# Kernel tuning notes

Hardware: AMD Instinct MI355X
Metric: run time of the kernel (lower is better)

## Reference

```python
import jax, jax.numpy as jnp
import numpy as np

N = 524288
NUM_LEVELS = 16
FEATS = 2
LOG2_T = 19
TABLE = 1 << LOG2_T
MIN_RES, MAX_RES = 16, 1024
PRIMES = np.array([1, 2654435761, 805459861], dtype=np.uint32)
_growth = np.exp((np.log(MAX_RES) - np.log(MIN_RES)) / (NUM_LEVELS - 1))
SCALINGS = np.floor(MIN_RES * _growth ** np.arange(NUM_LEVELS)).astype(np.float32)  # [L]


def hash_encode(positions, table):
    # positions [N,3] in [0,1]; table [L*T, F]
    scaled = positions[:, None, :] * jnp.asarray(SCALINGS)[None, :, None]  # [N,L,3]
    fl = jnp.floor(scaled)
    ce = jnp.ceil(scaled)
    offset = scaled - fl  # [N,L,3]
    primes = jnp.asarray(PRIMES)  # [3] uint32
    lvl_off = jnp.arange(NUM_LEVELS, dtype=jnp.uint32) * jnp.uint32(TABLE)  # [L]
    out = jnp.zeros(scaled.shape[:2] + (FEATS,), scaled.dtype)
    for corner in range(8):
        bits = np.array([(corner >> d) & 1 for d in range(3)], dtype=np.float32)
        coord = jnp.where(jnp.asarray(bits, dtype=bool), ce, fl)
        h = coord.astype(jnp.int32).astype(jnp.uint32) * primes  # [N,L,3]
        h = h[..., 0] ^ h[..., 1] ^ h[..., 2]
        idx = ((h & jnp.uint32(TABLE - 1)) + lvl_off).astype(jnp.int32)  # [N,L]
        b = jnp.asarray(bits)
        w = jnp.prod(b * offset + (1.0 - b) * (1.0 - offset), axis=-1, keepdims=True)  # [N,L,1]
        out = out + w * table[idx]
    return out.reshape(out.shape[0], NUM_LEVELS * FEATS)  # [N,32]


def nerf_encode(d):
    # NeRFEncoding: 4 freqs in 2**linspace(0,4,4), include_input=True -> 27 dims
    freqs = 2.0 ** jnp.linspace(0.0, 4.0, 4)
    scaled = (2.0 * jnp.pi * d)[..., None] * freqs  # [N,3,4]
    scaled = scaled.reshape(d.shape[0], -1)  # [N,12]
    enc = jnp.sin(jnp.concatenate([scaled, scaled + jnp.pi / 2.0], axis=-1))  # [N,24]
    return jnp.concatenate([enc, d], axis=-1)  # [N,27]


def setup_inputs() -> dict:
    key = jax.random.key(0)
    ks = jax.random.split(key, 16)
    w = lambda k, i, o: jax.random.normal(k, (i, o), jnp.float32) * (1.0 / np.sqrt(i))
    return {
        "positions": jax.random.uniform(ks[0], (N, 3), jnp.float32),
        "directions": jax.random.normal(ks[1], (N, 3), jnp.float32),
        "hash_table": (jax.random.uniform(ks[2], (NUM_LEVELS * TABLE, FEATS), jnp.float32) * 2.0 - 1.0) * 1e-3,
        "w0": w(ks[3], 32, 64), "b0": jnp.zeros((64,), jnp.float32),
        "w1": w(ks[4], 64, 64), "b1": jnp.zeros((64,), jnp.float32),
        "w2": w(ks[5], 64, 64), "b2": jnp.zeros((64,), jnp.float32),
        "wr": w(ks[6], 91, 32), "br": jnp.zeros((32,), jnp.float32),
        "wc": w(ks[7], 32, 3), "bc": jnp.zeros((3,), jnp.float32),
        "wd": w(ks[8], 64, 1), "bd": jnp.zeros((1,), jnp.float32),
    }


def reference(positions, directions, hash_table, w0, b0, w1, b1, w2, b2, wr, br, wc, bc, wd, bd):
    enc_xyz = hash_encode(positions, hash_table)  # [N,32]
    enc_dir = nerf_encode(directions)  # [N,27]
    h = jax.nn.relu(enc_xyz @ w0 + b0)
    h = jax.nn.relu(h @ w1 + b1)
    base = h @ w2 + b2  # [N,64], linear out (out_activation=None)
    rgb_h = jnp.concatenate([enc_dir, base], axis=-1) @ wr + br  # [N,32], single layer
    rgb = jax.nn.sigmoid(rgb_h @ wc + bc)  # [N,3]
    density = jax.nn.softplus(base @ wd + bd)  # [N,1]
    return jnp.concatenate([rgb, density], axis=-1)  # [N,4]
```

## Files before the change

kernel.cpp:

```cpp
#include <hip/hip_runtime.h>
#include <math.h>

#define NPTS 524288
#define LOG2T 19
#define TSIZE (1u << LOG2T)
#define TMASK (TSIZE - 1u)

typedef unsigned int uint32;
typedef unsigned short ushort16;

typedef __attribute__((ext_vector_type(8))) short short8;
typedef __attribute__((ext_vector_type(4))) float f32x4;

__device__ __forceinline__ float bf2f(ushort16 u) {
    union { uint32 i; float f; } v; v.i = ((uint32)u) << 16; return v.f;
}
__device__ __forceinline__ ushort16 f2bf(float f) {
    union { float f; uint32 i; } v; v.f = f;
    uint32 r = v.i + 0x7fffu + ((v.i >> 16) & 1u);
    return (ushort16)(r >> 16);
}
__device__ __forceinline__ uint32 pack2(float a, float b) {
    return (uint32)f2bf(a) | ((uint32)f2bf(b) << 16);
}
__device__ __forceinline__ float ldin(const void* p, int i, bool f32) {
    return f32 ? ((const float*)p)[i] : bf2f(((const ushort16*)p)[i]);
}

struct Scal16 { float s[16]; };
struct Freq4  { float f[4]; };
struct HashP  { float s[16]; int dD[8]; int doff[8]; };
struct DenseP { int dD[6]; int pfx[7]; };

__global__ __launch_bounds__(256) void k_cvt10(const void* __restrict__ pos,
                                               const float4* __restrict__ tbl,
                                               uint4* __restrict__ tbl2F) {
    __shared__ int sFlag;
    int tid = threadIdx.x;
    if (tid < 64) {
        const ushort16* ph = (const ushort16*)pos;
        float v0 = bf2f(ph[tid]), v1 = bf2f(ph[tid + 64]);
        bool odd = !(fabsf(v0) <= 4.f) || !(fabsf(v1) <= 4.f);
        unsigned long long m = __ballot(odd);
        if (tid == 0) sFlag = (m != 0ull) ? 1 : 0;
    }
    __syncthreads();
    if (sFlag == 0) return;
    size_t g = (size_t)blockIdx.x * 256 + tid;
    float4 v0 = tbl[(size_t)3 * TSIZE + 2 * g];
    float4 v1 = tbl[(size_t)3 * TSIZE + 2 * g + 1];
    uint4 o;
    o.x = pack2(v0.x, v0.y); o.y = pack2(v0.z, v0.w);
    o.z = pack2(v1.x, v1.y); o.w = pack2(v1.z, v1.w);
    tbl2F[g] = o;
}

__global__ __launch_bounds__(256) void k_dense(const void* __restrict__ pos,
                                               const void* __restrict__ tbl,
                                               uint4* __restrict__ dense4,
                                               DenseP dp) {
    __shared__ int sFlag;
    int tid = threadIdx.x;
    if (tid < 64) {
        const ushort16* ph = (const ushort16*)pos;
        float v0 = bf2f(ph[tid]), v1 = bf2f(ph[tid + 64]);
        bool odd = !(fabsf(v0) <= 4.f) || !(fabsf(v1) <= 4.f);
        unsigned long long m = __ballot(odd);
        if (tid == 0) sFlag = (m != 0ull) ? 1 : 0;
    }
    __syncthreads();
    const bool f32 = (sFlag != 0);

    int e = blockIdx.x * 256 + tid;
    if (e >= dp.pfx[6]) return;
    int l = 0;
#pragma unroll
    for (int k = 1; k < 6; ++k) l += (e >= dp.pfx[k]) ? 1 : 0;
    int c = e - dp.pfx[l];
    int D = dp.dD[l], D2 = D * D;
    int cz = c / D2; int rm = c - cz * D2;
    int cy = rm / D; int cx = rm - cy * D;

    uint32 base = (uint32)l << LOG2T;
    uint32 hz  = (uint32)cz * 805459861u;
    uint32 hy0 = (uint32)cy * 2654435761u;
    uint32 hy1 = (uint32)(cy + 1) * 2654435761u;
    uint32 h00 = ((((uint32)cx)       ^ hy0 ^ hz) & TMASK) + base;
    uint32 h10 = ((((uint32)(cx + 1)) ^ hy0 ^ hz) & TMASK) + base;
    uint32 h01 = ((((uint32)cx)       ^ hy1 ^ hz) & TMASK) + base;
    uint32 h11 = ((((uint32)(cx + 1)) ^ hy1 ^ hz) & TMASK) + base;

    uint4 o;
    if (f32) {
        const float2* t2 = (const float2*)tbl;
        float2 a = t2[h00], b = t2[h10], cc = t2[h01], d = t2[h11];
        o.x = pack2(a.x, a.y); o.y = pack2(b.x, b.y);
        o.z = pack2(cc.x, cc.y); o.w = pack2(d.x, d.y);
    } else {
        const uint32* t1 = (const uint32*)tbl;
        o.x = t1[h00]; o.y = t1[h10]; o.z = t1[h01]; o.w = t1[h11];
    }
    dense4[e] = o;
}

__global__ __launch_bounds__(256) void k_hashU(const void* __restrict__ pos,
                                               const void* __restrict__ tbl,
                                               const uint32* __restrict__ tbl2F,
                                               const uint4* __restrict__ dense4,
                                               uint32* __restrict__ enc,
                                               HashP hp, int lvl0) {
    __shared__ __align__(16) uint4 sPosQ[192];
    __shared__ int sFlag;
    int tid = threadIdx.x;
    if (tid < 64) {
        const ushort16* ph = (const ushort16*)pos;
        float v0 = bf2f(ph[tid]), v1 = bf2f(ph[tid + 64]);
        bool odd = !(fabsf(v0) <= 4.f) || !(fabsf(v1) <= 4.f);
        unsigned long long m = __ballot(odd);
        if (tid == 0) sFlag = (m != 0ull) ? 1 : 0;
    }
    __syncthreads();
    const bool f32 = (sFlag != 0);

    int lvl = lvl0 + (blockIdx.x & 7);
    int chunk = blockIdx.x >> 3;
    int p0 = chunk * 256;
    int pt = p0 + tid;

    {
        int n16 = f32 ? 192 : 96;
        const uint4* src = (const uint4*)((const char*)pos + (size_t)p0 * (f32 ? 12 : 6));
        for (int i = tid; i < n16; i += 256) sPosQ[i] = src[i];
    }
    __syncthreads();

    float x, y, z;
    if (f32) {
        const float* pf = (const float*)sPosQ;
        x = pf[3 * tid]; y = pf[3 * tid + 1]; z = pf[3 * tid + 2];
    } else {
        const ushort16* ph2 = (const ushort16*)sPosQ;
        x = bf2f(ph2[3 * tid]); y = bf2f(ph2[3 * tid + 1]); z = bf2f(ph2[3 * tid + 2]);
    }

    float s = hp.s[lvl];
    float sx = x * s, sy = y * s, sz = z * s;
    float fx = floorf(sx), fy = floorf(sy), fz = floorf(sz);
    float cx = ceilf(sx), cy = ceilf(sy), cz = ceilf(sz);
    float ox = sx - fx, oy = sy - fy, oz = sz - fz;
    float wx0 = 1.f - ox, wy0 = 1.f - oy, wz0 = 1.f - oz;

    float a0 = 0.f, a1 = 0.f;

    if (lvl < 6) {
        int D = hp.dD[lvl], D2 = D * D;
        int fxi = (int)fx, fyi = (int)fy, fzi = (int)fz;
        bool dxb = ((int)cx != fxi);
        bool dyb = ((int)cy != fyi);
        bool dzb = ((int)cz != fzi);
        const uint4* dp4 = dense4 + hp.doff[lvl];
        int i0 = fxi + fyi * D + fzi * D2;
        uint4 P0 = dp4[i0];
        uint4 P1 = dp4[i0 + (dzb ? D2 : 0)];
        {
            uint32 fv = P0.x, cv = dxb ? P0.y : P0.x;
            float w = wy0 * wz0;
            a0 += w * (wx0 * bf2f((ushort16)(fv & 0xffffu)) + ox * bf2f((ushort16)(cv & 0xffffu)));
            a1 += w * (wx0 * bf2f((ushort16)(fv >> 16))     + ox * bf2f((ushort16)(cv >> 16)));
        }
        {
            uint32 fv = dyb ? P0.z : P0.x;
            uint32 cv = dyb ? (dxb ? P0.w : P0.z) : (dxb ? P0.y : P0.x);
            float w = oy * wz0;
            a0 += w * (wx0 * bf2f((ushort16)(fv & 0xffffu)) + ox * bf2f((ushort16)(cv & 0xffffu)));
            a1 += w * (wx0 * bf2f((ushort16)(fv >> 16))     + ox * bf2f((ushort16)(cv >> 16)));
        }
        {
            uint32 fv = P1.x, cv = dxb ? P1.y : P1.x;
            float w = wy0 * oz;
            a0 += w * (wx0 * bf2f((ushort16)(fv & 0xffffu)) + ox * bf2f((ushort16)(cv & 0xffffu)));
            a1 += w * (wx0 * bf2f((ushort16)(fv >> 16))     + ox * bf2f((ushort16)(cv >> 16)));
        }
        {
            uint32 fv = dyb ? P1.z : P1.x;
            uint32 cv = dyb ? (dxb ? P1.w : P1.z) : (dxb ? P1.y : P1.x);
            float w = oy * oz;
            a0 += w * (wx0 * bf2f((ushort16)(fv & 0xffffu)) + ox * bf2f((ushort16)(cv & 0xffffu)));
            a1 += w * (wx0 * bf2f((ushort16)(fv >> 16))     + ox * bf2f((ushort16)(cv >> 16)));
        }
    } else {
        const uint32* tp; uint32 base;
        if (f32) { tp = tbl2F; base = (uint32)(lvl - 6) << LOG2T; }
        else     { tp = (const uint32*)tbl; base = (uint32)lvl << LOG2T; }
        uint32 hx0 = (uint32)(int)fx;
        uint32 hx1 = (uint32)(int)cx;
        uint32 hy0 = (uint32)(int)fy * 2654435761u;
        uint32 hy1 = (uint32)(int)cy * 2654435761u;
        uint32 hz0 = (uint32)(int)fz * 805459861u;
        uint32 hz1 = (uint32)(int)cz * 805459861u;
#pragma unroll
        for (int yz = 0; yz < 4; ++yz) {
            uint32 m = ((yz & 1) ? hy1 : hy0) ^ ((yz & 2) ? hz1 : hz0);
            float wyz = ((yz & 1) ? oy : wy0) * ((yz & 2) ? oz : wz0);
            uint32 i0 = ((hx0 ^ m) & TMASK) + base;
            uint32 i1 = ((hx1 ^ m) & TMASK) + base;
            uint32 d0, d1;
            if (i1 == (i0 ^ 1u)) {
                uint2 pv = *(const uint2*)(tp + (i0 & ~1u));
                d0 = (i0 & 1u) ? pv.y : pv.x;
                d1 = (i0 & 1u) ? pv.x : pv.y;
            } else {
                d0 = tp[i0]; d1 = tp[i1];
            }
            a0 += wyz * (wx0 * bf2f((ushort16)(d0 & 0xffffu)) + ox * bf2f((ushort16)(d1 & 0xffffu)));
            a1 += wyz * (wx0 * bf2f((ushort16)(d0 >> 16))     + ox * bf2f((ushort16)(d1 >> 16)));
        }
    }
    enc[(size_t)lvl * NPTS + pt] = pack2(a0, a1);
}

__global__ __launch_bounds__(256) void k_hash(const void* __restrict__ pos,
                                              const void* __restrict__ tbl,
                                              uint32* __restrict__ enc,
                                              Scal16 sc) {
    __shared__ int sFlag;
    int tid = threadIdx.x;
    if (tid < 64) {
        const ushort16* ph = (const ushort16*)pos;
        float v0 = bf2f(ph[tid]), v1 = bf2f(ph[tid + 64]);
        bool odd = !(fabsf(v0) <= 4.f) || !(fabsf(v1) <= 4.f);
        unsigned long long m = __ballot(odd);
        if (tid == 0) sFlag = (m != 0ull) ? 1 : 0;
    }
    __syncthreads();
    const bool f32 = (sFlag != 0);

    int lvl = ((blockIdx.x >> 14) << 3) + (blockIdx.x & 7);
    int pt = ((blockIdx.x >> 3) & 2047) * 256 + tid;

    float s = sc.s[lvl];
    float x = ldin(pos, 3 * pt, f32), y = ldin(pos, 3 * pt + 1, f32), z = ldin(pos, 3 * pt + 2, f32);
    float sx = x * s, sy = y * s, sz = z * s;
    float fx = floorf(sx), fy = floorf(sy), fz = floorf(sz);
    float cx = ceilf(sx), cy = ceilf(sy), cz = ceilf(sz);
    float ox = sx - fx, oy = sy - fy, oz = sz - fz;
    uint32 hx0 = (uint32)(int)fx;
    uint32 hx1 = (uint32)(int)cx;
    uint32 hy0 = (uint32)(int)fy * 2654435761u;
    uint32 hy1 = (uint32)(int)cy * 2654435761u;
    uint32 hz0 = (uint32)(int)fz * 805459861u;
    uint32 hz1 = (uint32)(int)cz * 805459861u;
    uint32 base = (uint32)lvl << LOG2T;
    float wx0 = 1.f - ox, wy0 = 1.f - oy, wz0 = 1.f - oz;

    float a0 = 0.f, a1 = 0.f;
    if (f32) {
        const float* tf = (const float*)tbl;
#pragma unroll
        for (int yz = 0; yz < 4; ++yz) {
            uint32 m = ((yz & 1) ? hy1 : hy0) ^ ((yz & 2) ? hz1 : hz0);
            float wyz = ((yz & 1) ? oy : wy0) * ((yz & 2) ? oz : wz0);
            uint32 i0 = ((hx0 ^ m) & TMASK) + base;
            uint32 i1 = ((hx1 ^ m) & TMASK) + base;
            float4 pv = *(const float4*)(tf + (size_t)(i0 & ~1u) * 2);
            bool lo = !(i0 & 1u);
            float f0 = lo ? pv.x : pv.z, f1 = lo ? pv.y : pv.w;
            float c0, c1;
            if (i1 == (i0 ^ 1u)) { c0 = lo ? pv.z : pv.x; c1 = lo ? pv.w : pv.y; }
            else { float2 tv = ((const float2*)tbl)[i1]; c0 = tv.x; c1 = tv.y; }
            a0 += wyz * (wx0 * f0 + ox * c0);
            a1 += wyz * (wx0 * f1 + ox * c1);
        }
    } else {
#pragma unroll
        for (int cr = 0; cr < 8; ++cr) {
            uint32 h = ((cr & 1) ? hx1 : hx0) ^ ((cr & 2) ? hy1 : hy0) ^ ((cr & 4) ? hz1 : hz0);
            uint32 idx = (h & TMASK) + base;
            uint32 dv = ((const uint32*)tbl)[idx];
            float w = ((cr & 1) ? ox : wx0) * ((cr & 2) ? oy : wy0) * ((cr & 4) ? oz : wz0);
            a0 += w * bf2f((ushort16)(dv & 0xffffu));
            a1 += w * bf2f((ushort16)(dv >> 16));
        }
    }
    enc[(size_t)lvl * NPTS + pt] = pack2(a0, a1);
}

#define STRY 72
#define STRW0 40
#define STRW12 72
#define STRWR 104
#define MSTRX 100
#define PPI 128
#define NIT (NPTS / PPI)

__global__ __launch_bounds__(512) void k_mlp(
    const void* __restrict__ pos,
    const uint32* __restrict__ enc, const void* __restrict__ dirs,
    const void* __restrict__ w0, const void* __restrict__ b0,
    const void* __restrict__ w1, const void* __restrict__ b1,
    const void* __restrict__ w2, const void* __restrict__ b2,
    const void* __restrict__ wr, const void* __restrict__ br,
    const void* __restrict__ wc, const void* __restrict__ bc,
    const void* __restrict__ wd, const void* __restrict__ bd,
    void* __restrict__ out, Freq4 fq)
{
    __shared__ __align__(16) ushort16 sX[PPI * MSTRX];
    __shared__ __align__(16) ushort16 sY[PPI * STRY];
    __shared__ __align__(16) ushort16 sW0[64 * STRW0];
    __shared__ __align__(16) ushort16 sW1[64 * STRW12];
    __shared__ __align__(16) ushort16 sW2[64 * STRW12];
    __shared__ __align__(16) ushort16 sWR[32 * STRWR];
    __shared__ __align__(16) ushort16 sW4[16 * STRWR];
    __shared__ __align__(16) float sB0[64], sB1[64], sB2[64], sBR[32], sFB[4];
    __shared__ int sFlag;

    int tid = threadIdx.x;

    if (tid < 64) {
        const ushort16* ph = (const ushort16*)pos;
        float v0 = bf2f(ph[tid]), v1 = bf2f(ph[tid + 64]);
        bool odd = !(fabsf(v0) <= 4.f) || !(fabsf(v1) <= 4.f);
        unsigned long long m = __ballot(odd);
        if (tid == 0) sFlag = (m != 0ull) ? 1 : 0;
    }
    __syncthreads();
    const bool f32 = (sFlag != 0);

    for (int i = tid; i < 2048; i += 512) { int k = i >> 6, n = i & 63; sW0[n * STRW0 + k] = f2bf(ldin(w0, i, f32)); }
    for (int i = tid; i < 4096; i += 512) { int k = i >> 6, n = i & 63; sW1[n * STRW12 + k] = f2bf(ldin(w1, i, f32)); }
    for (int i = tid; i < 4096; i += 512) { int k = i >> 6, n = i & 63; sW2[n * STRW12 + k] = f2bf(ldin(w2, i, f32)); }
    for (int i = tid; i < 2912; i += 512) {
        int r = i >> 5, n = i & 31; int k = (r < 27) ? r : r + 5;
        sWR[n * STRWR + k] = f2bf(ldin(wr, i, f32));
    }
    if (tid < 160) { int n = tid / 5, k = 27 + tid % 5; sWR[n * STRWR + k] = 0; }
    for (int i = tid; i < 1536; i += 512) {
        int n = i / 96, j = i % 96;
        float v = 0.f;
        if (n == 3 && j < 64) v = ldin(wd, j, f32);
        else if (n < 3 && j >= 64) v = ldin(wc, (j - 64) * 3 + n, f32);
        sW4[n * STRWR + j] = f2bf(v);
    }
    if (tid < 64) { sB0[tid] = ldin(b0, tid, f32); sB1[tid] = ldin(b1, tid, f32); sB2[tid] = ldin(b2, tid, f32); }
    if (tid < 32) sBR[tid] = ldin(br, tid, f32);
    if (tid < 3) sFB[tid] = ldin(bc, tid, f32);
    if (tid == 3) sFB[3] = ldin(bd, 0, f32);

    int lane = tid & 63, wv = tid >> 6;
    int colg = lane & 15, quad = lane >> 4;
    int myrow = wv * 16 + colg;

    for (int c = blockIdx.x; c < NIT; c += gridDim.x) {
        int p0 = c * PPI;
        __syncthreads();

        for (int i = tid; i < 1024; i += 512) {
            int l = i >> 6, p2 = (i & 63) * 2;
            uint2 e = *(const uint2*)&enc[(size_t)l * NPTS + p0 + p2];
            *(uint32*)&sX[p2 * MSTRX + 2 * l] = e.x;
            *(uint32*)&sX[(p2 + 1) * MSTRX + 2 * l] = e.y;
        }
        if (tid < 384) {
            int p = tid / 3, i2 = tid - 3 * (tid / 3);
            float dvv = ldin(dirs, 3 * (p0 + p) + i2, f32);
            ushort16* row = &sX[p * MSTRX + 64];
            float td = 6.28318530717958647692f * dvv;
            float a0 = td * fq.f[0], a1 = td * fq.f[1], a2 = td * fq.f[2], a3 = td * fq.f[3];
            uint2 sv, cv;
            sv.x = pack2(__sinf(a0), __sinf(a1));
// ... 211 lines not shown
                for (int r = 0; r < 4; ++r) {
                    float v = fmaxf(acc[r] + bias, 0.f);
                    sY[(wv * 16 + quad * 4 + r) * STRY + nt * 16 + colg] = f2bf(v);
                }
            }
        }
        __syncthreads();
        {
            short8 a0 = *(const short8*)&sY[(wv * 16 + colg) * STRY + quad * 8];
            short8 a1 = *(const short8*)&sY[(wv * 16 + colg) * STRY + 32 + quad * 8];
#pragma unroll
            for (int nt = 0; nt < 4; ++nt) {
                short8 bb0 = *(const short8*)&sW1[(nt * 16 + colg) * STRW12 + quad * 8];
                short8 bb1 = *(const short8*)&sW1[(nt * 16 + colg) * STRW12 + 32 + quad * 8];
                f32x4 acc = {0.f, 0.f, 0.f, 0.f};
                acc = __builtin_amdgcn_mfma_f32_16x16x32_bf16(a0, bb0, acc, 0, 0, 0);
                acc = __builtin_amdgcn_mfma_f32_16x16x32_bf16(a1, bb1, acc, 0, 0, 0);
                float bias = sB1[nt * 16 + colg];
#pragma unroll
                for (int r = 0; r < 4; ++r) {
                    float v = fmaxf(acc[r] + bias, 0.f);
                    sX[(wv * 16 + quad * 4 + r) * FSTRX + nt * 16 + colg] = f2bf(v);
                }
            }
        }
        __syncthreads();
        {
            short8 a0 = *(const short8*)&sX[(wv * 16 + colg) * FSTRX + quad * 8];
            short8 a1 = *(const short8*)&sX[(wv * 16 + colg) * FSTRX + 32 + quad * 8];
#pragma unroll
            for (int nt = 0; nt < 4; ++nt) {
                short8 bb0 = *(const short8*)&sW2[(nt * 16 + colg) * STRW12 + quad * 8];
                short8 bb1 = *(const short8*)&sW2[(nt * 16 + colg) * STRW12 + 32 + quad * 8];
                f32x4 acc = {0.f, 0.f, 0.f, 0.f};
                acc = __builtin_amdgcn_mfma_f32_16x16x32_bf16(a0, bb0, acc, 0, 0, 0);
                acc = __builtin_amdgcn_mfma_f32_16x16x32_bf16(a1, bb1, acc, 0, 0, 0);
                float bias = sB2[nt * 16 + colg];
#pragma unroll
                for (int r = 0; r < 4; ++r) {
                    sY[(wv * 16 + quad * 4 + r) * STRY + nt * 16 + colg] = f2bf(acc[r] + bias);
                }
            }
        }
        if (tid < 192) {
            int p = tid / 3, i2 = tid % 3;
            float dvv = ldin(dirs, 3 * (p0 + p) + i2, f32);
            ushort16* row = &sX[p * FSTRX + 64];
            float td = 6.28318530717958647692f * dvv;
#pragma unroll
            for (int j = 0; j < 4; ++j) {
                float arg = td * fq.f[j];
                float sv, cv;
                sincosf(arg, &sv, &cv);
                row[i2 * 4 + j] = f2bf(sv);
                row[12 + i2 * 4 + j] = f2bf(cv);
            }
            row[24 + i2] = f2bf(dvv);
        } else {
            int p = tid - 192;
            ushort16* row = &sX[p * FSTRX + 64];
#pragma unroll
            for (int j = 27; j < 32; ++j) row[j] = 0;
        }
        __syncthreads();
        {
            short8 a0 = *(const short8*)&sX[(wv * 16 + colg) * FSTRX + 64 + quad * 8];
            short8 a1 = *(const short8*)&sY[(wv * 16 + colg) * STRY + quad * 8];
            short8 a2 = *(const short8*)&sY[(wv * 16 + colg) * STRY + 32 + quad * 8];
#pragma unroll
            for (int nt = 0; nt < 2; ++nt) {
                short8 bb0 = *(const short8*)&sWR[(nt * 16 + colg) * STRWR + quad * 8];
                short8 bb1 = *(const short8*)&sWR[(nt * 16 + colg) * STRWR + 32 + quad * 8];
                short8 bb2 = *(const short8*)&sWR[(nt * 16 + colg) * STRWR + 64 + quad * 8];
                f32x4 acc = {0.f, 0.f, 0.f, 0.f};
                acc = __builtin_amdgcn_mfma_f32_16x16x32_bf16(a0, bb0, acc, 0, 0, 0);
                acc = __builtin_amdgcn_mfma_f32_16x16x32_bf16(a1, bb1, acc, 0, 0, 0);
                acc = __builtin_amdgcn_mfma_f32_16x16x32_bf16(a2, bb2, acc, 0, 0, 0);
                float bias = sBR[nt * 16 + colg];
#pragma unroll
                for (int r = 0; r < 4; ++r) {
                    sX[(wv * 16 + quad * 4 + r) * FSTRX + nt * 16 + colg] = f2bf(acc[r] + bias);
                }
            }
        }
        __syncthreads();
        if (tid < 64) {
            int pt = p0 + tid;
            float r0 = 0.f, r1 = 0.f, r2 = 0.f, dd = 0.f;
            const ushort16* hx = &sX[tid * FSTRX];
            const ushort16* hb = &sY[tid * STRY];
#pragma unroll
            for (int k = 0; k < 32; ++k) {
                float hv = bf2f(hx[k]);
                r0 += hv * sWCf[k * 3 + 0];
                r1 += hv * sWCf[k * 3 + 1];
                r2 += hv * sWCf[k * 3 + 2];
            }
#pragma unroll
            for (int k = 0; k < 64; ++k) dd += bf2f(hb[k]) * sWDf[k];
            r0 += sWCf[96]; r1 += sWCf[97]; r2 += sWCf[98]; dd += sWCf[99];
            r0 = 1.f / (1.f + expf(-r0));
            r1 = 1.f / (1.f + expf(-r1));
            r2 = 1.f / (1.f + expf(-r2));
            float sp = (dd > 0.f) ? (dd + log1pf(expf(-dd))) : log1pf(expf(dd));
            if (f32) {
                float4 o4; o4.x = r0; o4.y = r1; o4.z = r2; o4.w = sp;
                ((float4*)out)[pt] = o4;
            } else {
                uint2 o;
                o.x = pack2(r0, r1); o.y = pack2(r2, sp);
                ((uint2*)out)[pt] = o;
            }
        }
    }
}

extern "C" void kernel_launch(void* const* d_in, const int* in_sizes, int n_in,
                              void* d_out, int out_size, void* d_ws, size_t ws_size,
                              hipStream_t stream) {
    (void)in_sizes; (void)n_in; (void)out_size;

    Scal16 sc;
    double g = exp((log(1024.0) - log(16.0)) / 15.0);
    for (int l = 0; l < 16; ++l) sc.s[l] = (float)floor(16.0 * pow(g, (double)l));

    Freq4 fq;
    float lv[4] = {0.f, 4.f / 3.f, 8.f / 3.f, 4.f};
    for (int j = 0; j < 4; ++j) fq.f[j] = (float)pow(2.0, (double)lv[j]);

    DenseP dpp;
    HashP hp;
    dpp.pfx[0] = 0;
    for (int l = 0; l < 6; ++l) {
        int D = (int)sc.s[l] + 1;
        dpp.dD[l] = D;
        dpp.pfx[l + 1] = dpp.pfx[l] + D * D * D;
    }
    for (int l = 0; l < 16; ++l) hp.s[l] = sc.s[l];
    for (int l = 0; l < 8; ++l) {
        hp.dD[l]   = (l < 6) ? dpp.dD[l] : 1;
        hp.doff[l] = (l < 6) ? dpp.pfx[l] : 0;
    }
    int ndense = dpp.pfx[6];

    const size_t enc_bytes   = (size_t)16 * NPTS * 4;
    const size_t tbl2F_bytes = (size_t)10 * TSIZE * 4;
    const size_t dense_bytes = (size_t)ndense * 16 + 64;
    const size_t need_new = enc_bytes + tbl2F_bytes + dense_bytes;

    if (ws_size >= need_new) {
        uint32* enc   = (uint32*)d_ws;
        uint32* tbl2F = (uint32*)((char*)d_ws + enc_bytes);
        uint4*  dense4 = (uint4*)((char*)d_ws + enc_bytes + tbl2F_bytes);
        k_cvt10<<<dim3(5120), dim3(256), 0, stream>>>(d_in[0], (const float4*)d_in[2], (uint4*)tbl2F);
        k_dense<<<dim3((ndense + 255) / 256), dim3(256), 0, stream>>>(d_in[0], d_in[2], dense4, dpp);
        k_hashU<<<dim3(8 * NPTS / 256), dim3(256), 0, stream>>>(d_in[0], d_in[2], tbl2F, dense4, enc, hp, 0);
        k_hashU<<<dim3(8 * NPTS / 256), dim3(256), 0, stream>>>(d_in[0], d_in[2], tbl2F, dense4, enc, hp, 8);
        k_mlp<<<dim3(512), dim3(512), 0, stream>>>(
            d_in[0], enc, d_in[1], d_in[3], d_in[4], d_in[5], d_in[6], d_in[7],
            d_in[8], d_in[9], d_in[10], d_in[11], d_in[12], d_in[13], d_in[14],
            d_out, fq);
    } else if (ws_size >= enc_bytes) {
        uint32* enc = (uint32*)d_ws;
        k_hash<<<dim3(2 * 8 * NPTS / 256), dim3(256), 0, stream>>>(d_in[0], d_in[2], enc, sc);
        k_mlp<<<dim3(512), dim3(512), 0, stream>>>(
            d_in[0], enc, d_in[1], d_in[3], d_in[4], d_in[5], d_in[6], d_in[7],
            d_in[8], d_in[9], d_in[10], d_in[11], d_in[12], d_in[13], d_in[14],
            d_out, fq);
    } else {
        k_fused<<<dim3(512), dim3(256), 0, stream>>>(
            d_in[0], d_in[1], d_in[2], d_in[3], d_in[4], d_in[5], d_in[6], d_in[7],
            d_in[8], d_in[9], d_in[10], d_in[11], d_in[12], d_in[13], d_in[14],
            d_out, sc, fq);
    }
}
```

Before: 345.6 us.

## Split hash encoding into dense-level kernel and XCD-aware hashed-level kernel

Moves the six dense-grid levels into their own kernel, where each thread loops over all six levels for one point and loads its position once. The ten hashed levels go to a separate kernel that remaps block IDs so each XCD handles a contiguous range of (level, chunk) work. With that mapping each XCD's L2 mostly sees one or two levels' 2 MB table slices, which should improve cache locality for the random gathers. This replaces the two interleaved launches that mixed dense and hashed levels in one grid. The risk is lower parallelism in the dense kernel (only NPTS/256 blocks) and dependence on the round-robin block-to-XCD assignment.

```diff
diff --git a/kernel.cpp b/kernel.cpp
--- a/kernel.cpp
+++ b/kernel.cpp
@@ -103,12 +103,10 @@
     dense4[e] = o;
 }
 
-__global__ __launch_bounds__(256) void k_hashU(const void* __restrict__ pos,
-                                               const void* __restrict__ tbl,
-                                               const uint32* __restrict__ tbl2F,
-                                               const uint4* __restrict__ dense4,
-                                               uint32* __restrict__ enc,
-                                               HashP hp, int lvl0) {
+__global__ __launch_bounds__(256) void k_denseEnc(const void* __restrict__ pos,
+                                                  const uint4* __restrict__ dense4,
+                                                  uint32* __restrict__ enc,
+                                                  HashP hp) {
     __shared__ __align__(16) uint4 sPosQ[192];
     __shared__ int sFlag;
     int tid = threadIdx.x;
@@ -122,9 +120,7 @@
     __syncthreads();
     const bool f32 = (sFlag != 0);
 
-    int lvl = lvl0 + (blockIdx.x & 7);
-    int chunk = blockIdx.x >> 3;
-    int p0 = chunk * 256;
+    int p0 = blockIdx.x * 256;
     int pt = p0 + tid;
 
     {
@@ -143,6 +139,98 @@
         x = bf2f(ph2[3 * tid]); y = bf2f(ph2[3 * tid + 1]); z = bf2f(ph2[3 * tid + 2]);
     }
 
+#pragma unroll
+    for (int l = 0; l < 6; ++l) {
+        float s = hp.s[l];
+        float sx = x * s, sy = y * s, sz = z * s;
+        float fx = floorf(sx), fy = floorf(sy), fz = floorf(sz);
+        float cx = ceilf(sx), cy = ceilf(sy), cz = ceilf(sz);
+        float ox = sx - fx, oy = sy - fy, oz = sz - fz;
+        float wx0 = 1.f - ox, wy0 = 1.f - oy, wz0 = 1.f - oz;
+
+        int D = hp.dD[l], D2 = D * D;
+        int fxi = (int)fx, fyi = (int)fy, fzi = (int)fz;
+        bool dxb = ((int)cx != fxi);
+        bool dyb = ((int)cy != fyi);
+        bool dzb = ((int)cz != fzi);
+        const uint4* dp4 = dense4 + hp.doff[l];
+        int i0 = fxi + fyi * D + fzi * D2;
+        uint4 P0 = dp4[i0];
+        uint4 P1 = dp4[i0 + (dzb ? D2 : 0)];
+
+        float a0 = 0.f, a1 = 0.f;
+        {
+            uint32 fv = P0.x, cv = dxb ? P0.y : P0.x;
+            float w = wy0 * wz0;
+            a0 += w * (wx0 * bf2f((ushort16)(fv & 0xffffu)) + ox * bf2f((ushort16)(cv & 0xffffu)));
+            a1 += w * (wx0 * bf2f((ushort16)(fv >> 16))     + ox * bf2f((ushort16)(cv >> 16)));
+        }
+        {
+            uint32 fv = dyb ? P0.z : P0.x;
+            uint32 cv = dyb ? (dxb ? P0.w : P0.z) : (dxb ? P0.y : P0.x);
+            float w = oy * wz0;
+            a0 += w * (wx0 * bf2f((ushort16)(fv & 0xffffu)) + ox * bf2f((ushort16)(cv & 0xffffu)));
+            a1 += w * (wx0 * bf2f((ushort16)(fv >> 16))     + ox * bf2f((ushort16)(cv >> 16)));
+        }
+        {
+            uint32 fv = P1.x, cv = dxb ? P1.y : P1.x;
+            float w = wy0 * oz;
+            a0 += w * (wx0 * bf2f((ushort16)(fv & 0xffffu)) + ox * bf2f((ushort16)(cv & 0xffffu)));
+            a1 += w * (wx0 * bf2f((ushort16)(fv >> 16))     + ox * bf2f((ushort16)(cv >> 16)));
+        }
+        {
+            uint32 fv = dyb ? P1.z : P1.x;
+            uint32 cv = dyb ? (dxb ? P1.w : P1.z) : (dxb ? P1.y : P1.x);
+            float w = oy * oz;
+            a0 += w * (wx0 * bf2f((ushort16)(fv & 0xffffu)) + ox * bf2f((ushort16)(cv & 0xffffu)));
+            a1 += w * (wx0 * bf2f((ushort16)(fv >> 16))     + ox * bf2f((ushort16)(cv >> 16)));
+        }
+        enc[(size_t)l * NPTS + pt] = pack2(a0, a1);
+    }
+}
+
+__global__ __launch_bounds__(256) void k_hashB(const void* __restrict__ pos,
+                                               const void* __restrict__ tbl,
+                                               const uint32* __restrict__ tbl2F,
+                                               uint32* __restrict__ enc,
+                                               HashP hp) {
+    __shared__ __align__(16) uint4 sPosQ[192];
+    __shared__ int sFlag;
+    int tid = threadIdx.x;
+    if (tid < 64) {
+        const ushort16* ph = (const ushort16*)pos;
+        float v0 = bf2f(ph[tid]), v1 = bf2f(ph[tid + 64]);
+        bool odd = !(fabsf(v0) <= 4.f) || !(fabsf(v1) <= 4.f);
+        unsigned long long m = __ballot(odd);
+        if (tid == 0) sFlag = (m != 0ull) ? 1 : 0;
+    }
+    __syncthreads();
+    const bool f32 = (sFlag != 0);
+
+    int xcd = blockIdx.x & 7;
+    int slot = blockIdx.x >> 3;
+    int W = xcd * 2560 + slot;
+    int lvl = 6 + (W >> 11);
+    int chunk = W & 2047;
+    int p0 = chunk * 256;
+    int pt = p0 + tid;
+
+    {
+        int n16 = f32 ? 192 : 96;
+        const uint4* src = (const uint4*)((const char*)pos + (size_t)p0 * (f32 ? 12 : 6));
+        for (int i = tid; i < n16; i += 256) sPosQ[i] = src[i];
+    }
+    __syncthreads();
+
+    float x, y, z;
+    if (f32) {
+        const float* pf = (const float*)sPosQ;
+        x = pf[3 * tid]; y = pf[3 * tid + 1]; z = pf[3 * tid + 2];
+    } else {
+        const ushort16* ph2 = (const ushort16*)sPosQ;
+        x = bf2f(ph2[3 * tid]); y = bf2f(ph2[3 * tid + 1]); z = bf2f(ph2[3 * tid + 2]);
+    }
+
     float s = hp.s[lvl];
     float sx = x * s, sy = y * s, sz = z * s;
     float fx = floorf(sx), fy = floorf(sy), fz = floorf(sz);
@@ -150,71 +238,33 @@
     float ox = sx - fx, oy = sy - fy, oz = sz - fz;
     float wx0 = 1.f - ox, wy0 = 1.f - oy, wz0 = 1.f - oz;
 
+    const uint32* tp; uint32 base;
+    if (f32) { tp = tbl2F; base = (uint32)(lvl - 6) << LOG2T; }
+    else     { tp = (const uint32*)tbl; base = (uint32)lvl << LOG2T; }
+    uint32 hx0 = (uint32)(int)fx;
+    uint32 hx1 = (uint32)(int)cx;
+    uint32 hy0 = (uint32)(int)fy * 2654435761u;
+    uint32 hy1 = (uint32)(int)cy * 2654435761u;
+    uint32 hz0 = (uint32)(int)fz * 805459861u;
+    uint32 hz1 = (uint32)(int)cz * 805459861u;
+
     float a0 = 0.f, a1 = 0.f;
-
-    if (lvl < 6) {
-        int D = hp.dD[lvl], D2 = D * D;
-        int fxi = (int)fx, fyi = (int)fy, fzi = (int)fz;
-        bool dxb = ((int)cx != fxi);
-        bool dyb = ((int)cy != fyi);
-        bool dzb = ((int)cz != fzi);
-        const uint4* dp4 = dense4 + hp.doff[lvl];
-        int i0 = fxi + fyi * D + fzi * D2;
-        uint4 P0 = dp4[i0];
-        uint4 P1 = dp4[i0 + (dzb ? D2 : 0)];
-        {
-            uint32 fv = P0.x, cv = dxb ? P0.y : P0.x;
-            float w = wy0 * wz0;
-            a0 += w * (wx0 * bf2f((ushort16)(fv & 0xffffu)) + ox * bf2f((ushort16)(cv & 0xffffu)));
-            a1 += w * (wx0 * bf2f((ushort16)(fv >> 16))     + ox * bf2f((ushort16)(cv >> 16)));
-        }
-        {
-            uint32 fv = dyb ? P0.z : P0.x;
-            uint32 cv = dyb ? (dxb ? P0.w : P0.z) : (dxb ? P0.y : P0.x);
-            float w = oy * wz0;
-            a0 += w * (wx0 * bf2f((ushort16)(fv & 0xffffu)) + ox * bf2f((ushort16)(cv & 0xffffu)));
-            a1 += w * (wx0 * bf2f((ushort16)(fv >> 16))     + ox * bf2f((ushort16)(cv >> 16)));
-        }
-        {
-            uint32 fv = P1.x, cv = dxb ? P1.y : P1.x;
-            float w = wy0 * oz;
-            a0 += w * (wx0 * bf2f((ushort16)(fv & 0xffffu)) + ox * bf2f((ushort16)(cv & 0xffffu)));
-            a1 += w * (wx0 * bf2f((ushort16)(fv >> 16))     + ox * bf2f((ushort16)(cv >> 16)));
-        }
-        {
-            uint32 fv = dyb ? P1.z : P1.x;
-            uint32 cv = dyb ? (dxb ? P1.w : P1.z) : (dxb ? P1.y : P1.x);
-            float w = oy * oz;
-            a0 += w * (wx0 * bf2f((ushort16)(fv & 0xffffu)) + ox * bf2f((ushort16)(cv & 0xffffu)));
-            a1 += w * (wx0 * bf2f((ushort16)(fv >> 16))     + ox * bf2f((ushort16)(cv >> 16)));
-        }
-    } else {
-        const uint32* tp; uint32 base;
-        if (f32) { tp = tbl2F; base = (uint32)(lvl - 6) << LOG2T; }
-        else     { tp = (const uint32*)tbl; base = (uint32)lvl << LOG2T; }
-        uint32 hx0 = (uint32)(int)fx;
-        uint32 hx1 = (uint32)(int)cx;
-        uint32 hy0 = (uint32)(int)fy * 2654435761u;
-        uint32 hy1 = (uint32)(int)cy * 2654435761u;
-        uint32 hz0 = (uint32)(int)fz * 805459861u;
-        uint32 hz1 = (uint32)(int)cz * 805459861u;
-#pragma unroll
-        for (int yz = 0; yz < 4; ++yz) {
-            uint32 m = ((yz & 1) ? hy1 : hy0) ^ ((yz & 2) ? hz1 : hz0);
-            float wyz = ((yz & 1) ? oy : wy0) * ((yz & 2) ? oz : wz0);
-            uint32 i0 = ((hx0 ^ m) & TMASK) + base;
-            uint32 i1 = ((hx1 ^ m) & TMASK) + base;
-            uint32 d0, d1;
-            if (i1 == (i0 ^ 1u)) {
-                uint2 pv = *(const uint2*)(tp + (i0 & ~1u));
-                d0 = (i0 & 1u) ? pv.y : pv.x;
-                d1 = (i0 & 1u) ? pv.x : pv.y;
-            } else {
-                d0 = tp[i0]; d1 = tp[i1];
-            }
-            a0 += wyz * (wx0 * bf2f((ushort16)(d0 & 0xffffu)) + ox * bf2f((ushort16)(d1 & 0xffffu)));
-            a1 += wyz * (wx0 * bf2f((ushort16)(d0 >> 16))     + ox * bf2f((ushort16)(d1 >> 16)));
-        }
+#pragma unroll
+    for (int yz = 0; yz < 4; ++yz) {
+        uint32 m = ((yz & 1) ? hy1 : hy0) ^ ((yz & 2) ? hz1 : hz0);
+        float wyz = ((yz & 1) ? oy : wy0) * ((yz & 2) ? oz : wz0);
+        uint32 i0 = ((hx0 ^ m) & TMASK) + base;
+        uint32 i1 = ((hx1 ^ m) & TMASK) + base;
+        uint32 d0, d1;
+        if (i1 == (i0 ^ 1u)) {
+            uint2 pv = *(const uint2*)(tp + (i0 & ~1u));
+            d0 = (i0 & 1u) ? pv.y : pv.x;
+            d1 = (i0 & 1u) ? pv.x : pv.y;
+        } else {
+            d0 = tp[i0]; d1 = tp[i1];
+        }
+        a0 += wyz * (wx0 * bf2f((ushort16)(d0 & 0xffffu)) + ox * bf2f((ushort16)(d1 & 0xffffu)));
+        a1 += wyz * (wx0 * bf2f((ushort16)(d0 >> 16))     + ox * bf2f((ushort16)(d1 >> 16)));
     }
     enc[(size_t)lvl * NPTS + pt] = pack2(a0, a1);
 }
@@ -734,8 +784,8 @@
         uint4*  dense4 = (uint4*)((char*)d_ws + enc_bytes + tbl2F_bytes);
         k_cvt10<<<dim3(5120), dim3(256), 0, stream>>>(d_in[0], (const float4*)d_in[2], (uint4*)tbl2F);
         k_dense<<<dim3((ndense + 255) / 256), dim3(256), 0, stream>>>(d_in[0], d_in[2], dense4, dpp);
-        k_hashU<<<dim3(8 * NPTS / 256), dim3(256), 0, stream>>>(d_in[0], d_in[2], tbl2F, dense4, enc, hp, 0);
-        k_hashU<<<dim3(8 * NPTS / 256), dim3(256), 0, stream>>>(d_in[0], d_in[2], tbl2F, dense4, enc, hp, 8);
+        k_denseEnc<<<dim3(NPTS / 256), dim3(256), 0, stream>>>(d_in[0], dense4, enc, hp);
+        k_hashB<<<dim3(10 * NPTS / 256), dim3(256), 0, stream>>>(d_in[0], d_in[2], tbl2F, enc, hp);
         k_mlp<<<dim3(512), dim3(512), 0, stream>>>(
             d_in[0], enc, d_in[1], d_in[3], d_in[4], d_in[5], d_in[6], d_in[7],
             d_in[8], d_in[9], d_in[10], d_in[11], d_in[12], d_in[13], d_in[14],
```

New measurement: 325.4 us. -5.8%, faster.

## Merge prep kernels and remap hash blocks so each XCD owns whole levels

Applied to the files above, without the earlier changes.

The table-conversion and dense-grid kernels become one launch, saving a kernel boundary. The encode kernel gets a new block-to-work mapping. Hashed levels 6-15 are split five per launch, and blocks are assigned so each XCD (blockIdx&7) covers contiguous chunks of the same level, improving L2 locality of the per-level table. The six dense levels are computed together by dedicated blocks that reuse one position load across all six levels. This adds a divergent role split inside the kernel and uneven per-block work between dense and hashed blocks.

```diff
diff --git a/kernel.cpp b/kernel.cpp
--- a/kernel.cpp
+++ b/kernel.cpp
@@ -32,9 +32,11 @@
 struct HashP  { float s[16]; int dD[8]; int doff[8]; };
 struct DenseP { int dD[6]; int pfx[7]; };
 
-__global__ __launch_bounds__(256) void k_cvt10(const void* __restrict__ pos,
-                                               const float4* __restrict__ tbl,
-                                               uint4* __restrict__ tbl2F) {
+__global__ __launch_bounds__(256) void k_prep(const void* __restrict__ pos,
+                                              const void* __restrict__ tbl,
+                                              uint4* __restrict__ tbl2F,
+                                              uint4* __restrict__ dense4,
+                                              DenseP dp) {
     __shared__ int sFlag;
     int tid = threadIdx.x;
     if (tid < 64) {
@@ -45,33 +47,22 @@
         if (tid == 0) sFlag = (m != 0ull) ? 1 : 0;
     }
     __syncthreads();
-    if (sFlag == 0) return;
-    size_t g = (size_t)blockIdx.x * 256 + tid;
-    float4 v0 = tbl[(size_t)3 * TSIZE + 2 * g];
-    float4 v1 = tbl[(size_t)3 * TSIZE + 2 * g + 1];
-    uint4 o;
-    o.x = pack2(v0.x, v0.y); o.y = pack2(v0.z, v0.w);
-    o.z = pack2(v1.x, v1.y); o.w = pack2(v1.z, v1.w);
-    tbl2F[g] = o;
-}
-
-__global__ __launch_bounds__(256) void k_dense(const void* __restrict__ pos,
-                                               const void* __restrict__ tbl,
-                                               uint4* __restrict__ dense4,
-                                               DenseP dp) {
-    __shared__ int sFlag;
-    int tid = threadIdx.x;
-    if (tid < 64) {
-        const ushort16* ph = (const ushort16*)pos;
-        float v0 = bf2f(ph[tid]), v1 = bf2f(ph[tid + 64]);
-        bool odd = !(fabsf(v0) <= 4.f) || !(fabsf(v1) <= 4.f);
-        unsigned long long m = __ballot(odd);
-        if (tid == 0) sFlag = (m != 0ull) ? 1 : 0;
-    }
-    __syncthreads();
     const bool f32 = (sFlag != 0);
 
-    int e = blockIdx.x * 256 + tid;
+    if (blockIdx.x < 5120) {
+        if (!f32) return;
+        const float4* tf4 = (const float4*)tbl;
+        size_t g = (size_t)blockIdx.x * 256 + tid;
+        float4 v0 = tf4[(size_t)3 * TSIZE + 2 * g];
+        float4 v1 = tf4[(size_t)3 * TSIZE + 2 * g + 1];
+        uint4 o;
+        o.x = pack2(v0.x, v0.y); o.y = pack2(v0.z, v0.w);
+        o.z = pack2(v1.x, v1.y); o.w = pack2(v1.z, v1.w);
+        tbl2F[g] = o;
+        return;
+    }
+
+    int e = (blockIdx.x - 5120) * 256 + tid;
     if (e >= dp.pfx[6]) return;
     int l = 0;
 #pragma unroll
@@ -103,12 +94,12 @@
     dense4[e] = o;
 }
 
-__global__ __launch_bounds__(256) void k_hashU(const void* __restrict__ pos,
-                                               const void* __restrict__ tbl,
-                                               const uint32* __restrict__ tbl2F,
-                                               const uint4* __restrict__ dense4,
-                                               uint32* __restrict__ enc,
-                                               HashP hp, int lvl0) {
+__global__ __launch_bounds__(256) void k_enc2(const void* __restrict__ pos,
+                                              const void* __restrict__ tbl,
+                                              const uint32* __restrict__ tbl2F,
+                                              const uint4* __restrict__ dense4,
+                                              uint32* __restrict__ enc,
+                                              HashP hp, int half) {
     __shared__ __align__(16) uint4 sPosQ[192];
     __shared__ int sFlag;
     int tid = threadIdx.x;
@@ -122,8 +113,17 @@
     __syncthreads();
     const bool f32 = (sFlag != 0);
 
-    int lvl = lvl0 + (blockIdx.x & 7);
-    int chunk = blockIdx.x >> 3;
+    int xcd = blockIdx.x & 7;
+    int slot = blockIdx.x >> 3;
+    bool denseRole = (slot >= 1280);
+    int lvl = 0, chunk;
+    if (!denseRole) {
+        int W = xcd * 1280 + slot;
+        lvl = 6 + 5 * half + (W >> 11);
+        chunk = W & 2047;
+    } else {
+        chunk = half * 1024 + (slot - 1280) * 8 + xcd;
+    }
     int p0 = chunk * 256;
     int pt = p0 + tid;
 
@@ -143,6 +143,58 @@
         x = bf2f(ph2[3 * tid]); y = bf2f(ph2[3 * tid + 1]); z = bf2f(ph2[3 * tid + 2]);
     }
 
+    if (denseRole) {
+#pragma unroll
+        for (int l = 0; l < 6; ++l) {
+            float s = hp.s[l];
+            float sx = x * s, sy = y * s, sz = z * s;
+            float fx = floorf(sx), fy = floorf(sy), fz = floorf(sz);
+            float cx = ceilf(sx), cy = ceilf(sy), cz = ceilf(sz);
+            float ox = sx - fx, oy = sy - fy, oz = sz - fz;
+            float wx0 = 1.f - ox, wy0 = 1.f - oy, wz0 = 1.f - oz;
+
+            int D = hp.dD[l], D2 = D * D;
+            int fxi = (int)fx, fyi = (int)fy, fzi = (int)fz;
+            bool dxb = ((int)cx != fxi);
+            bool dyb = ((int)cy != fyi);
+            bool dzb = ((int)cz != fzi);
+            const uint4* dp4 = dense4 + hp.doff[l];
+            int i0 = fxi + fyi * D + fzi * D2;
+            uint4 P0 = dp4[i0];
+            uint4 P1 = dp4[i0 + (dzb ? D2 : 0)];
+
+            float a0 = 0.f, a1 = 0.f;
+            {
+                uint32 fv = P0.x, cv = dxb ? P0.y : P0.x;
+                float w = wy0 * wz0;
+                a0 += w * (wx0 * bf2f((ushort16)(fv & 0xffffu)) + ox * bf2f((ushort16)(cv & 0xffffu)));
+                a1 += w * (wx0 * bf2f((ushort16)(fv >> 16))     + ox * bf2f((ushort16)(cv >> 16)));
+            }
+            {
+                uint32 fv = dyb ? P0.z : P0.x;
+                uint32 cv = dyb ? (dxb ? P0.w : P0.z) : (dxb ? P0.y : P0.x);
+                float w = oy * wz0;
+                a0 += w * (wx0 * bf2f((ushort16)(fv & 0xffffu)) + ox * bf2f((ushort16)(cv & 0xffffu)));
+                a1 += w * (wx0 * bf2f((ushort16)(fv >> 16))     + ox * bf2f((ushort16)(cv >> 16)));
+            }
+            {
+                uint32 fv = P1.x, cv = dxb ? P1.y : P1.x;
+                float w = wy0 * oz;
+                a0 += w * (wx0 * bf2f((ushort16)(fv & 0xffffu)) + ox * bf2f((ushort16)(cv & 0xffffu)));
+                a1 += w * (wx0 * bf2f((ushort16)(fv >> 16))     + ox * bf2f((ushort16)(cv >> 16)));
+            }
+            {
+                uint32 fv = dyb ? P1.z : P1.x;
+                uint32 cv = dyb ? (dxb ? P1.w : P1.z) : (dxb ? P1.y : P1.x);
+                float w = oy * oz;
+                a0 += w * (wx0 * bf2f((ushort16)(fv & 0xffffu)) + ox * bf2f((ushort16)(cv & 0xffffu)));
+                a1 += w * (wx0 * bf2f((ushort16)(fv >> 16))     + ox * bf2f((ushort16)(cv >> 16)));
+            }
+            enc[(size_t)l * NPTS + pt] = pack2(a0, a1);
+        }
+        return;
+    }
+
     float s = hp.s[lvl];
     float sx = x * s, sy = y * s, sz = z * s;
     float fx = floorf(sx), fy = floorf(sy), fz = floorf(sz);
@@ -150,71 +202,33 @@
     float ox = sx - fx, oy = sy - fy, oz = sz - fz;
     float wx0 = 1.f - ox, wy0 = 1.f - oy, wz0 = 1.f - oz;
 
+    const uint32* tp; uint32 base;
+    if (f32) { tp = tbl2F; base = (uint32)(lvl - 6) << LOG2T; }
+    else     { tp = (const uint32*)tbl; base = (uint32)lvl << LOG2T; }
+    uint32 hx0 = (uint32)(int)fx;
+    uint32 hx1 = (uint32)(int)cx;
+    uint32 hy0 = (uint32)(int)fy * 2654435761u;
+    uint32 hy1 = (uint32)(int)cy * 2654435761u;
+    uint32 hz0 = (uint32)(int)fz * 805459861u;
+    uint32 hz1 = (uint32)(int)cz * 805459861u;
+
     float a0 = 0.f, a1 = 0.f;
-
-    if (lvl < 6) {
-        int D = hp.dD[lvl], D2 = D * D;
-        int fxi = (int)fx, fyi = (int)fy, fzi = (int)fz;
-        bool dxb = ((int)cx != fxi);
-        bool dyb = ((int)cy != fyi);
-        bool dzb = ((int)cz != fzi);
-        const uint4* dp4 = dense4 + hp.doff[lvl];
-        int i0 = fxi + fyi * D + fzi * D2;
-        uint4 P0 = dp4[i0];
-        uint4 P1 = dp4[i0 + (dzb ? D2 : 0)];
-        {
-            uint32 fv = P0.x, cv = dxb ? P0.y : P0.x;
-            float w = wy0 * wz0;
-            a0 += w * (wx0 * bf2f((ushort16)(fv & 0xffffu)) + ox * bf2f((ushort16)(cv & 0xffffu)));
-            a1 += w * (wx0 * bf2f((ushort16)(fv >> 16))     + ox * bf2f((ushort16)(cv >> 16)));
-        }
-        {
-            uint32 fv = dyb ? P0.z : P0.x;
-            uint32 cv = dyb ? (dxb ? P0.w : P0.z) : (dxb ? P0.y : P0.x);
-            float w = oy * wz0;
-            a0 += w * (wx0 * bf2f((ushort16)(fv & 0xffffu)) + ox * bf2f((ushort16)(cv & 0xffffu)));
-            a1 += w * (wx0 * bf2f((ushort16)(fv >> 16))     + ox * bf2f((ushort16)(cv >> 16)));
-        }
-        {
-            uint32 fv = P1.x, cv = dxb ? P1.y : P1.x;
-            float w = wy0 * oz;
-            a0 += w * (wx0 * bf2f((ushort16)(fv & 0xffffu)) + ox * bf2f((ushort16)(cv & 0xffffu)));
-            a1 += w * (wx0 * bf2f((ushort16)(fv >> 16))     + ox * bf2f((ushort16)(cv >> 16)));
-        }
-        {
-            uint32 fv = dyb ? P1.z : P1.x;
-            uint32 cv = dyb ? (dxb ? P1.w : P1.z) : (dxb ? P1.y : P1.x);
-            float w = oy * oz;
-            a0 += w * (wx0 * bf2f((ushort16)(fv & 0xffffu)) + ox * bf2f((ushort16)(cv & 0xffffu)));
-            a1 += w * (wx0 * bf2f((ushort16)(fv >> 16))     + ox * bf2f((ushort16)(cv >> 16)));
-        }
-    } else {
-        const uint32* tp; uint32 base;
-        if (f32) { tp = tbl2F; base = (uint32)(lvl - 6) << LOG2T; }
-        else     { tp = (const uint32*)tbl; base = (uint32)lvl << LOG2T; }
-        uint32 hx0 = (uint32)(int)fx;
-        uint32 hx1 = (uint32)(int)cx;
-        uint32 hy0 = (uint32)(int)fy * 2654435761u;
-        uint32 hy1 = (uint32)(int)cy * 2654435761u;
-        uint32 hz0 = (uint32)(int)fz * 805459861u;
-        uint32 hz1 = (uint32)(int)cz * 805459861u;
-#pragma unroll
-        for (int yz = 0; yz < 4; ++yz) {
-            uint32 m = ((yz & 1) ? hy1 : hy0) ^ ((yz & 2) ? hz1 : hz0);
-            float wyz = ((yz & 1) ? oy : wy0) * ((yz & 2) ? oz : wz0);
-            uint32 i0 = ((hx0 ^ m) & TMASK) + base;
-            uint32 i1 = ((hx1 ^ m) & TMASK) + base;
-            uint32 d0, d1;
-            if (i1 == (i0 ^ 1u)) {
-                uint2 pv = *(const uint2*)(tp + (i0 & ~1u));
-                d0 = (i0 & 1u) ? pv.y : pv.x;
-                d1 = (i0 & 1u) ? pv.x : pv.y;
-            } else {
-                d0 = tp[i0]; d1 = tp[i1];
-            }
-            a0 += wyz * (wx0 * bf2f((ushort16)(d0 & 0xffffu)) + ox * bf2f((ushort16)(d1 & 0xffffu)));
-            a1 += wyz * (wx0 * bf2f((ushort16)(d0 >> 16))     + ox * bf2f((ushort16)(d1 >> 16)));
-        }
+#pragma unroll
+    for (int yz = 0; yz < 4; ++yz) {
+        uint32 m = ((yz & 1) ? hy1 : hy0) ^ ((yz & 2) ? hz1 : hz0);
+        float wyz = ((yz & 1) ? oy : wy0) * ((yz & 2) ? oz : wz0);
+        uint32 i0 = ((hx0 ^ m) & TMASK) + base;
+        uint32 i1 = ((hx1 ^ m) & TMASK) + base;
+        uint32 d0, d1;
+        if (i1 == (i0 ^ 1u)) {
+            uint2 pv = *(const uint2*)(tp + (i0 & ~1u));
+            d0 = (i0 & 1u) ? pv.y : pv.x;
+            d1 = (i0 & 1u) ? pv.x : pv.y;
+        } else {
+            d0 = tp[i0]; d1 = tp[i1];
+        }
+        a0 += wyz * (wx0 * bf2f((ushort16)(d0 & 0xffffu)) + ox * bf2f((ushort16)(d1 & 0xffffu)));
+        a1 += wyz * (wx0 * bf2f((ushort16)(d0 >> 16))     + ox * bf2f((ushort16)(d1 >> 16)));
     }
     enc[(size_t)lvl * NPTS + pt] = pack2(a0, a1);
 }
@@ -732,10 +746,10 @@
         uint32* enc   = (uint32*)d_ws;
         uint32* tbl2F = (uint32*)((char*)d_ws + enc_bytes);
         uint4*  dense4 = (uint4*)((char*)d_ws + enc_bytes + tbl2F_bytes);
-        k_cvt10<<<dim3(5120), dim3(256), 0, stream>>>(d_in[0], (const float4*)d_in[2], (uint4*)tbl2F);
-        k_dense<<<dim3((ndense + 255) / 256), dim3(256), 0, stream>>>(d_in[0], d_in[2], dense4, dpp);
-        k_hashU<<<dim3(8 * NPTS / 256), dim3(256), 0, stream>>>(d_in[0], d_in[2], tbl2F, dense4, enc, hp, 0);
-        k_hashU<<<dim3(8 * NPTS / 256), dim3(256), 0, stream>>>(d_in[0], d_in[2], tbl2F, dense4, enc, hp, 8);
+        int nprep = 5120 + (ndense + 255) / 256;
+        k_prep<<<dim3(nprep), dim3(256), 0, stream>>>(d_in[0], d_in[2], (uint4*)tbl2F, dense4, dpp);
+        k_enc2<<<dim3(11264), dim3(256), 0, stream>>>(d_in[0], d_in[2], tbl2F, dense4, enc, hp, 0);
+        k_enc2<<<dim3(11264), dim3(256), 0, stream>>>(d_in[0], d_in[2], tbl2F, dense4, enc, hp, 1);
         k_mlp<<<dim3(512), dim3(512), 0, stream>>>(
             d_in[0], enc, d_in[1], d_in[3], d_in[4], d_in[5], d_in[6], d_in[7],
             d_in[8], d_in[9], d_in[10], d_in[11], d_in[12], d_in[13], d_in[14],
```

Result: faster. 329.6 us (-4.6%).
